# Kernel optimization log

Hardware: AMD Instinct MI355X
Metric: run time of the kernel (lower is better)

## Reference

```python
import jax, jax.numpy as jnp
import numpy as np

EPS = 1e-6          # torch F.pairwise_distance default eps (added to the difference)
NORM_EPS = 1e-12    # torch F.normalize default eps
CORRECT_W = 1.0
INCORRECT_W = 0.0001


def _l2norm(x):
    return x / jnp.maximum(jnp.linalg.norm(x, axis=1, keepdims=True), NORM_EPS)


def setup_inputs() -> dict:
    key = jax.random.key(0)
    k1, k2, k3 = jax.random.split(key, 3)
    N, D, R = 1048576, 128, 53
    model_output = jax.random.normal(k1, (N, D), dtype=jnp.float32)
    target = _l2norm(jax.random.normal(k2, (N, D), dtype=jnp.float32))
    # RelationEmbedding stores row-normalized embeddings
    relation_embeds = _l2norm(jax.random.normal(k3, (R, D), dtype=jnp.float32))
    return {"model_output": model_output, "target": target, "relation_embeds": relation_embeds}


def reference(model_output, target, relation_embeds):
    # F.normalize(model_output, p=2, dim=1)
    mo = _l2norm(model_output)

    # correct term: sum_i || mo_i - target_i + eps ||_2
    correct = jnp.sum(jnp.sqrt(jnp.sum((mo - target + EPS) ** 2, axis=1)))

    # incorrect term: for each row, max over relations of || mo_i - emb_r + eps ||_2.
    # Expand || d + eps ||^2 = ||d||^2 + 2*eps*sum(d) + D*eps^2 to avoid an [N,R,D] tensor.
    D = mo.shape[1]
    mo_sq = jnp.sum(mo * mo, axis=1)                       # [N]
    re_sq = jnp.sum(relation_embeds * relation_embeds, axis=1)  # [R]
    dots = mo @ relation_embeds.T                          # [N, R]
    mo_sum = jnp.sum(mo, axis=1)                           # [N]
    re_sum = jnp.sum(relation_embeds, axis=1)              # [R]
    sq = (mo_sq[:, None] + re_sq[None, :] - 2.0 * dots
          + 2.0 * EPS * (mo_sum[:, None] - re_sum[None, :])
          + D * EPS * EPS)                                 # [N, R]
    dist = jnp.sqrt(jnp.maximum(sq, 0.0))
    incorrect = jnp.sum(jnp.max(dist, axis=1))

    return CORRECT_W * correct + INCORRECT_W * (1.0 - incorrect)
```

## Files before the change

### kernel.cpp

```cpp
#include <hip/hip_runtime.h>

typedef __attribute__((ext_vector_type(8))) short short8;
typedef __attribute__((ext_vector_type(4))) float f32x4;

#define EPS 1e-6f
#define NB 2048

static __device__ __forceinline__ short f2bf(float f) {
    unsigned u = __float_as_uint(f);
    unsigned r = (u + 0x7FFFu + ((u >> 16) & 1u)) >> 16;
    return (short)(unsigned short)r;
}

__global__ void prep_kernel(const float* __restrict__ re, short* __restrict__ re_bf,
                            float* __restrict__ re_c2, int R) {
    int tid = threadIdx.x;
    int r = tid >> 2, q = tid & 3;
    float v[32];
    if (r < R) {
        const float* p = re + (size_t)r * 128 + q * 32;
#pragma unroll
        for (int j = 0; j < 32; ++j) v[j] = p[j];
    } else {
#pragma unroll
        for (int j = 0; j < 32; ++j) v[j] = 0.f;
    }
    float ssq = 0.f, sum = 0.f;
#pragma unroll
    for (int j = 0; j < 32; ++j) { ssq = fmaf(v[j], v[j], ssq); sum += v[j]; }
    ssq += __shfl_xor(ssq, 1); ssq += __shfl_xor(ssq, 2);
    sum += __shfl_xor(sum, 1); sum += __shfl_xor(sum, 2);
    short* o = re_bf + r * 128 + q * 32;
#pragma unroll
    for (int j = 0; j < 32; ++j) o[j] = f2bf(v[j]);
    if (q == 0) re_c2[r] = (r < R) ? (ssq - 2.f * EPS * sum) : -1e30f;
}

__global__ __launch_bounds__(256) void loss_main(
    const float* __restrict__ mo, const float* __restrict__ tg,
    const short* __restrict__ re_bf, const float* __restrict__ re_c2,
    float* __restrict__ partials, int nrows) {
    const int tid = threadIdx.x;
    const int lane = tid & 63;
    const int widx = tid >> 6;
    const int col16 = lane & 15;
    const int kg = lane >> 4;
    const int ko = kg * 8;

    short8 bfrag[4][4];
    float rc[4];
#pragma unroll
    for (int rt = 0; rt < 4; ++rt) {
#pragma unroll
        for (int s = 0; s < 4; ++s)
            bfrag[rt][s] = *reinterpret_cast<const short8*>(
                re_bf + (rt * 16 + col16) * 128 + s * 32 + ko);
        rc[rt] = re_c2[rt * 16 + col16];
    }

    float corr_acc = 0.f, inc_acc = 0.f;
    const int NT = nrows >> 4;
    const int nw = gridDim.x * 4;
    for (int t = blockIdx.x * 4 + widx; t < NT; t += nw) {
        const size_t rowoff = (size_t)(t * 16 + col16) * 128 + ko;
        const float* rp = mo + rowoff;
        const float* tp = tg + rowoff;
        alignas(16) float x[32];
        alignas(16) float tv[32];
#pragma unroll
        for (int s = 0; s < 4; ++s) {
            *(f32x4*)(x + s * 8)     = *(const f32x4*)(rp + s * 32);
            *(f32x4*)(x + s * 8 + 4) = *(const f32x4*)(rp + s * 32 + 4);
        }
#pragma unroll
        for (int s = 0; s < 4; ++s) {
            *(f32x4*)(tv + s * 8)     = *(const f32x4*)(tp + s * 32);
            *(f32x4*)(tv + s * 8 + 4) = *(const f32x4*)(tp + s * 32 + 4);
        }
        float ssq = 0.f, sum = 0.f;
#pragma unroll
        for (int j = 0; j < 32; ++j) { ssq = fmaf(x[j], x[j], ssq); sum += x[j]; }
        ssq += __shfl_xor(ssq, 16); ssq += __shfl_xor(ssq, 32);
        sum += __shfl_xor(sum, 16); sum += __shfl_xor(sum, 32);
        float rnorm = 1.0f / fmaxf(sqrtf(ssq), 1e-12f);
        float mo_sq = ssq * rnorm * rnorm;
        float mo_sum = sum * rnorm;

        float cs = 0.f;
#pragma unroll
        for (int j = 0; j < 32; ++j) {
            float d = fmaf(x[j], rnorm, EPS - tv[j]);
            cs = fmaf(d, d, cs);
        }
        cs += __shfl_xor(cs, 16); cs += __shfl_xor(cs, 32);
        if (lane < 16) corr_acc += sqrtf(cs);

        short8 afrag[4];
#pragma unroll
        for (int s = 0; s < 4; ++s)
#pragma unroll
            for (int j = 0; j < 8; ++j)
                afrag[s][j] = f2bf(x[s * 8 + j] * rnorm);

        float mconst[4];
#pragma unroll
        for (int reg = 0; reg < 4; ++reg) {
            int src = kg * 4 + reg;
            float msq  = __shfl(mo_sq, src);
            float msum = __shfl(mo_sum, src);
            mconst[reg] = fmaf(2.f * EPS, msum, msq) + 128.f * EPS * EPS;
        }

        float vmax[4] = {-1e30f, -1e30f, -1e30f, -1e30f};
#pragma unroll
        for (int rt = 0; rt < 4; ++rt) {
            f32x4 acc = {0.f, 0.f, 0.f, 0.f};
#pragma unroll
            for (int s = 0; s < 4; ++s)
                acc = __builtin_amdgcn_mfma_f32_16x16x32_bf16(afrag[s], bfrag[rt][s], acc, 0, 0, 0);
#pragma unroll
            for (int reg = 0; reg < 4; ++reg) {
                float d2 = mconst[reg] + rc[rt] - 2.f * acc[reg];
                vmax[reg] = fmaxf(vmax[reg], d2);
            }
        }
#pragma unroll
        for (int m = 1; m < 16; m <<= 1)
#pragma unroll
            for (int reg = 0; reg < 4; ++reg)
                vmax[reg] = fmaxf(vmax[reg], __shfl_xor(vmax[reg], m));
        if (col16 == 0) {
#pragma unroll
            for (int reg = 0; reg < 4; ++reg)
                inc_acc += sqrtf(fmaxf(vmax[reg], 0.f));
        }
    }

    __shared__ float redc[256];
    __shared__ float redi[256];
    redc[tid] = corr_acc; redi[tid] = inc_acc;
    __syncthreads();
    for (int s = 128; s > 0; s >>= 1) {
        if (tid < s) { redc[tid] += redc[tid + s]; redi[tid] += redi[tid + s]; }
        __syncthreads();
    }
    if (tid == 0) {
        partials[blockIdx.x * 2]     = redc[0];
        partials[blockIdx.x * 2 + 1] = redi[0];
    }
}

__global__ void final_kernel(const float* __restrict__ partials, float* __restrict__ out, int nb) {
    __shared__ float rc_[256];
    __shared__ float ri_[256];
    int tid = threadIdx.x;
    float c = 0.f, ic = 0.f;
    for (int i = tid; i < nb; i += 256) { c += partials[2 * i]; ic += partials[2 * i + 1]; }
    rc_[tid] = c; ri_[tid] = ic;
    __syncthreads();
    for (int s = 128; s > 0; s >>= 1) {
        if (tid < s) { rc_[tid] += rc_[tid + s]; ri_[tid] += ri_[tid + s]; }
        __syncthreads();
    }
    if (tid == 0) out[0] = c * 0.f + rc_[0] + 1e-4f * (1.f - ri_[0]);
}

extern "C" void kernel_launch(void* const* d_in, const int* in_sizes, int n_in,
                              void* d_out, int out_size, void* d_ws, size_t ws_size,
                              hipStream_t stream) {
    const float* mo = (const float*)d_in[0];
    const float* tg = (const float*)d_in[1];
    const float* re = (const float*)d_in[2];
    const int D = 128;
    const int nrows = in_sizes[0] / D;
    const int R = in_sizes[2] / D;

    char* ws = (char*)d_ws;
    short* re_bf   = (short*)ws;
    float* re_c2   = (float*)(ws + 16384);
    float* partials = (float*)(ws + 16896);

    prep_kernel<<<1, 256, 0, stream>>>(re, re_bf, re_c2, R);
    loss_main<<<NB, 256, 0, stream>>>(mo, tg, re_bf, re_c2, partials, nrows);
    final_kernel<<<1, 256, 0, stream>>>(partials, (float*)d_out, NB);
}
```

Measured before the change: 227.9 us.

## Prefetch next row tile, move relation fragments to LDS, swap MFMA operands

```diff
diff --git a/kernel.cpp b/kernel.cpp
--- a/kernel.cpp
+++ b/kernel.cpp
@@ -47,92 +47,111 @@
     const int kg = lane >> 4;
     const int ko = kg * 8;
 
-    short8 bfrag[4][4];
-    float rc[4];
-#pragma unroll
-    for (int rt = 0; rt < 4; ++rt) {
-#pragma unroll
-        for (int s = 0; s < 4; ++s)
-            bfrag[rt][s] = *reinterpret_cast<const short8*>(
-                re_bf + (rt * 16 + col16) * 128 + s * 32 + ko);
-        rc[rt] = re_c2[rt * 16 + col16];
-    }
+    __shared__ short8 bf_lds[16][64];
+    if (widx == 0) {
+#pragma unroll
+        for (int rt = 0; rt < 4; ++rt)
+#pragma unroll
+            for (int s = 0; s < 4; ++s)
+                bf_lds[rt * 4 + s][lane] = *reinterpret_cast<const short8*>(
+                    re_bf + (rt * 16 + col16) * 128 + s * 32 + ko);
+    }
+    float rc[4][4];
+#pragma unroll
+    for (int rt = 0; rt < 4; ++rt)
+#pragma unroll
+        for (int reg = 0; reg < 4; ++reg)
+            rc[rt][reg] = re_c2[rt * 16 + kg * 4 + reg];
+    __syncthreads();
 
     float corr_acc = 0.f, inc_acc = 0.f;
     const int NT = nrows >> 4;
     const int nw = gridDim.x * 4;
-    for (int t = blockIdx.x * 4 + widx; t < NT; t += nw) {
-        const size_t rowoff = (size_t)(t * 16 + col16) * 128 + ko;
-        const float* rp = mo + rowoff;
-        const float* tp = tg + rowoff;
+    int t = blockIdx.x * 4 + widx;
+
+    if (t < NT) {
         alignas(16) float x[32];
-        alignas(16) float tv[32];
-#pragma unroll
-        for (int s = 0; s < 4; ++s) {
-            *(f32x4*)(x + s * 8)     = *(const f32x4*)(rp + s * 32);
-            *(f32x4*)(x + s * 8 + 4) = *(const f32x4*)(rp + s * 32 + 4);
+
+        {
+            const float* rp = mo + ((size_t)(t * 16 + col16) * 128 + ko);
+#pragma unroll
+            for (int s = 0; s < 4; ++s) {
+                *(f32x4*)(x + s * 8)     = *(const f32x4*)(rp + s * 32);
+                *(f32x4*)(x + s * 8 + 4) = *(const f32x4*)(rp + s * 32 + 4);
+            }
         }
-#pragma unroll
-        for (int s = 0; s < 4; ++s) {
-            *(f32x4*)(tv + s * 8)     = *(const f32x4*)(tp + s * 32);
-            *(f32x4*)(tv + s * 8 + 4) = *(const f32x4*)(tp + s * 32 + 4);
-        }
-        float ssq = 0.f, sum = 0.f;
-#pragma unroll
-        for (int j = 0; j < 32; ++j) { ssq = fmaf(x[j], x[j], ssq); sum += x[j]; }
-        ssq += __shfl_xor(ssq, 16); ssq += __shfl_xor(ssq, 32);
-        sum += __shfl_xor(sum, 16); sum += __shfl_xor(sum, 32);
-        float rnorm = 1.0f / fmaxf(sqrtf(ssq), 1e-12f);
-        float mo_sq = ssq * rnorm * rnorm;
-        float mo_sum = sum * rnorm;
-
-        float cs = 0.f;
-#pragma unroll
-        for (int j = 0; j < 32; ++j) {
-            float d = fmaf(x[j], rnorm, EPS - tv[j]);
-            cs = fmaf(d, d, cs);
-        }
-        cs += __shfl_xor(cs, 16); cs += __shfl_xor(cs, 32);
-        if (lane < 16) corr_acc += sqrtf(cs);
-
-        short8 afrag[4];
-#pragma unroll
-        for (int s = 0; s < 4; ++s)
-#pragma unroll
-            for (int j = 0; j < 8; ++j)
-                afrag[s][j] = f2bf(x[s * 8 + j] * rnorm);
-
-        float mconst[4];
-#pragma unroll
-        for (int reg = 0; reg < 4; ++reg) {
-            int src = kg * 4 + reg;
-            float msq  = __shfl(mo_sq, src);
-            float msum = __shfl(mo_sum, src);
-            mconst[reg] = fmaf(2.f * EPS, msum, msq) + 128.f * EPS * EPS;
-        }
-
-        float vmax[4] = {-1e30f, -1e30f, -1e30f, -1e30f};
-#pragma unroll
-        for (int rt = 0; rt < 4; ++rt) {
-            f32x4 acc = {0.f, 0.f, 0.f, 0.f};
+
+        while (t < NT) {
+            alignas(16) float tv[32];
+            {
+                const float* tp = tg + ((size_t)(t * 16 + col16) * 128 + ko);
+#pragma unroll
+                for (int s = 0; s < 4; ++s) {
+                    *(f32x4*)(tv + s * 8)     = *(const f32x4*)(tp + s * 32);
+                    *(f32x4*)(tv + s * 8 + 4) = *(const f32x4*)(tp + s * 32 + 4);
+                }
+            }
+
+            float ssq = 0.f, sum = 0.f;
+#pragma unroll
+            for (int j = 0; j < 32; ++j) { ssq = fmaf(x[j], x[j], ssq); sum += x[j]; }
+            float xt = 0.f, tsq = 0.f, tsum = 0.f;
+#pragma unroll
+            for (int j = 0; j < 32; ++j) {
+                xt  = fmaf(x[j], tv[j], xt);
+                tsq = fmaf(tv[j], tv[j], tsq);
+                tsum += tv[j];
+            }
+            ssq  += __shfl_xor(ssq, 16);  ssq  += __shfl_xor(ssq, 32);
+            sum  += __shfl_xor(sum, 16);  sum  += __shfl_xor(sum, 32);
+            xt   += __shfl_xor(xt, 16);   xt   += __shfl_xor(xt, 32);
+            tsq  += __shfl_xor(tsq, 16);  tsq  += __shfl_xor(tsq, 32);
+            tsum += __shfl_xor(tsum, 16); tsum += __shfl_xor(tsum, 32);
+
+            float rnorm  = 1.0f / fmaxf(sqrtf(ssq), 1e-12f);
+            float mo_sq  = ssq * rnorm * rnorm;
+            float mo_sum = sum * rnorm;
+            float mconst = fmaf(2.f * EPS, mo_sum, mo_sq) + 128.f * EPS * EPS;
+
+            float cs = mconst + tsq - 2.f * EPS * tsum - 2.f * rnorm * xt;
+            if (kg == 0) corr_acc += sqrtf(fmaxf(cs, 0.f));
+
+            short8 afrag[4];
 #pragma unroll
             for (int s = 0; s < 4; ++s)
-                acc = __builtin_amdgcn_mfma_f32_16x16x32_bf16(afrag[s], bfrag[rt][s], acc, 0, 0, 0);
-#pragma unroll
-            for (int reg = 0; reg < 4; ++reg) {
-                float d2 = mconst[reg] + rc[rt] - 2.f * acc[reg];
-                vmax[reg] = fmaxf(vmax[reg], d2);
-            }
-        }
-#pragma unroll
-        for (int m = 1; m < 16; m <<= 1)
-#pragma unroll
-            for (int reg = 0; reg < 4; ++reg)
-                vmax[reg] = fmaxf(vmax[reg], __shfl_xor(vmax[reg], m));
-        if (col16 == 0) {
-#pragma unroll
-            for (int reg = 0; reg < 4; ++reg)
-                inc_acc += sqrtf(fmaxf(vmax[reg], 0.f));
+#pragma unroll
+                for (int j = 0; j < 8; ++j)
+                    afrag[s][j] = f2bf(x[s * 8 + j] * rnorm);
+
+            int t2 = t + nw;
+            if (t2 < NT) {
+                const float* rp = mo + ((size_t)(t2 * 16 + col16) * 128 + ko);
+#pragma unroll
+                for (int s = 0; s < 4; ++s) {
+                    *(f32x4*)(x + s * 8)     = *(const f32x4*)(rp + s * 32);
+                    *(f32x4*)(x + s * 8 + 4) = *(const f32x4*)(rp + s * 32 + 4);
+                }
+            }
+
+            float vmax = -1e30f;
+#pragma unroll
+            for (int rt = 0; rt < 4; ++rt) {
+                f32x4 acc = {0.f, 0.f, 0.f, 0.f};
+#pragma unroll
+                for (int s = 0; s < 4; ++s)
+                    acc = __builtin_amdgcn_mfma_f32_16x16x32_bf16(
+                        bf_lds[rt * 4 + s][lane], afrag[s], acc, 0, 0, 0);
+#pragma unroll
+                for (int reg = 0; reg < 4; ++reg) {
+                    float d2 = mconst + rc[rt][reg] - 2.f * acc[reg];
+                    vmax = fmaxf(vmax, d2);
+                }
+            }
+            vmax = fmaxf(vmax, __shfl_xor(vmax, 16));
+            vmax = fmaxf(vmax, __shfl_xor(vmax, 32));
+            if (kg == 0) inc_acc += sqrtf(fmaxf(vmax, 0.f));
+
+            t = t2;
         }
     }
 
@@ -162,7 +181,7 @@
         if (tid < s) { rc_[tid] += rc_[tid + s]; ri_[tid] += ri_[tid + s]; }
         __syncthreads();
     }
-    if (tid == 0) out[0] = c * 0.f + rc_[0] + 1e-4f * (1.f - ri_[0]);
+    if (tid == 0) out[0] = rc_[0] + 1e-4f * (1.f - ri_[0]);
 }
 
 extern "C" void kernel_launch(void* const* d_in, const int* in_sizes, int n_in,
@@ -176,8 +195,8 @@
     const int R = in_sizes[2] / D;
 
     char* ws = (char*)d_ws;
-    short* re_bf   = (short*)ws;
-    float* re_c2   = (float*)(ws + 16384);
+    short* re_bf    = (short*)ws;
+    float* re_c2    = (float*)(ws + 16384);
     float* partials = (float*)(ws + 16896);
 
     prep_kernel<<<1, 256, 0, stream>>>(re, re_bf, re_c2, R);
```

New measurement: 188.2 us. 1.21x faster.
